# Kernel optimization log

Measured on AMD Instinct MI355X. Metric: run time of the kernel, lower is better.

The kernel has to match this reference:

```python
import jax, jax.numpy as jnp
import numpy as np

N = 100000      # nodes
E = 1600000     # edges (avg degree 16)
IN_FEATS = 128
HEADS = 4
OUT_FEATS = 16
NEG_SLOPE = 0.2
EPS = 1e-16


def setup_inputs() -> dict:
    key = jax.random.key(0)
    k1, k2, k3, k4, k5, k6 = jax.random.split(key, 6)
    feat = jax.random.normal(k1, (N, IN_FEATS), dtype=jnp.float32)
    # xavier-ish scale for params
    W = jax.random.normal(k2, (IN_FEATS, HEADS * OUT_FEATS), dtype=jnp.float32) * 0.1
    attn_l = jax.random.normal(k3, (1, HEADS, OUT_FEATS), dtype=jnp.float32) * 0.1
    attn_r = jax.random.normal(k4, (1, HEADS, OUT_FEATS), dtype=jnp.float32) * 0.1
    src_index = jax.random.randint(k5, (E,), 0, N, dtype=jnp.int32)
    trg_index = jax.random.randint(k6, (E,), 0, N, dtype=jnp.int32)
    return {"feat": feat, "W": W, "attn_l": attn_l, "attn_r": attn_r,
            "src_index": src_index, "trg_index": trg_index}


def reference(feat, W, attn_l, attn_r, src_index, trg_index):
    # dropout layers are identity in eval mode
    n = feat.shape[0]
    h = (feat @ W).reshape(n, HEADS, OUT_FEATS)            # [N,H,F]
    el = jnp.sum(h * attn_l, axis=-1)                      # [N,H]
    er = jnp.sum(h * attn_r, axis=-1)                      # [N,H]
    s = el[src_index] + er[trg_index]                      # [E,H] edge scores
    s = jnp.where(s > 0, s, NEG_SLOPE * s)                 # LeakyReLU(0.2)
    # neighborhood-aware softmax over incoming edges of each target node
    s = s - jnp.max(s)                                     # global max shift (as in source)
    e = jnp.exp(s)                                         # [E,H]
    denom = jax.ops.segment_sum(e, trg_index, num_segments=n)  # [N,H]
    attn = e / (denom[trg_index] + EPS)                    # [E,H]
    # weighted aggregation of lifted source features into target nodes
    msg = h[src_index] * attn[:, :, None]                  # [E,H,F]
    h_prime = jax.ops.segment_sum(msg, trg_index, num_segments=n)  # [N,H,F]
    return h_prime.reshape(n, HEADS * OUT_FEATS)
```

## Files before the change

kernel.cpp:

```cpp
#include <hip/hip_runtime.h>

typedef unsigned short ushort_t;
typedef __attribute__((ext_vector_type(8))) short bf16x8;
typedef __attribute__((ext_vector_type(4))) float f32x4v;

#define EPB 8000

static __device__ __forceinline__ float bf2f(ushort_t u) {
  union { unsigned int i; float f; } v; v.i = ((unsigned int)u) << 16; return v.f;
}
static __device__ __forceinline__ ushort_t f2bf(float f) {
  union { float f; unsigned int i; } v; v.f = f;
  unsigned int r = v.i + 0x7FFFu + ((v.i >> 16) & 1u);
  return (ushort_t)(r >> 16);
}
static __device__ __forceinline__ short f2bfs(float f) {
  return (short)f2bf(f);
}
static __device__ __forceinline__ float leaky(float s) {
  return s > 0.f ? s : 0.2f * s;
}

__global__ __launch_bounds__(256) void gat_packw(
    const float* __restrict__ W, ushort_t* __restrict__ wfrag)
{
  const int t = threadIdx.x;
  const int w = t >> 6, l = t & 63;
  const int q = l >> 4, n = l & 15;
  #pragma unroll
  for (int kc = 0; kc < 4; ++kc) {
    #pragma unroll
    for (int j = 0; j < 8; ++j) {
      const int k = kc * 32 + q * 8 + j;
      wfrag[(((w * 4 + kc) * 64) + l) * 8 + j] = f2bf(W[k * 64 + w * 16 + n]);
    }
  }
}

__global__ __launch_bounds__(256) void gat_linear(
    const float* __restrict__ feat, const ushort_t* __restrict__ wfrag,
    const float* __restrict__ attnl, const float* __restrict__ attnr,
    ushort_t* __restrict__ h_out, float* __restrict__ el, float* __restrict__ er,
    float* __restrict__ blockmax2, int N)
{
  __shared__ float sF[16 * 132];
  __shared__ float wmax[8];
  const int t = threadIdx.x;
  const int b = blockIdx.x;
  const int w = t >> 6, l = t & 63;
  const int q = l >> 4, m = l & 15;

  bf16x8 bfr[4];
  #pragma unroll
  for (int kc = 0; kc < 4; ++kc)
    bfr[kc] = *(const bf16x8*)(wfrag + (((w * 4 + kc) * 64) + l) * 8);

  const float al = attnl[w * 16 + m];
  const float ar = attnr[w * 16 + m];

  const float4* gF = (const float4*)(feat + (size_t)b * 16 * 128);
  #pragma unroll
  for (int i = 0; i < 2; ++i) {
    const int idx = i * 256 + t;
    const int node = idx >> 5, off = idx & 31;
    float4 v = make_float4(0.f, 0.f, 0.f, 0.f);
    if (b * 16 + node < N) v = gF[idx];
    *(float4*)(sF + node * 132 + off * 4) = v;
  }
  __syncthreads();

  f32x4v acc = {0.f, 0.f, 0.f, 0.f};
  const float* arow = sF + m * 132 + q * 8;
  #pragma unroll
  for (int kc = 0; kc < 4; ++kc) {
    const float4 a0 = *(const float4*)(arow + kc * 32);
    const float4 a1 = *(const float4*)(arow + kc * 32 + 4);
    bf16x8 af;
    af[0] = f2bfs(a0.x); af[1] = f2bfs(a0.y);
    af[2] = f2bfs(a0.z); af[3] = f2bfs(a0.w);
    af[4] = f2bfs(a1.x); af[5] = f2bfs(a1.y);
    af[6] = f2bfs(a1.z); af[7] = f2bfs(a1.w);
    acc = __builtin_amdgcn_mfma_f32_16x16x32_bf16(af, bfr[kc], acc, 0, 0, 0);
  }

  float mel = -1e30f, mer = -1e30f;
  #pragma unroll
  for (int r = 0; r < 4; ++r) {
    const int node = q * 4 + r;
    const int gn = b * 16 + node;
    const float hv = acc[r];
    float evl = hv * al;
    float evr = hv * ar;
    #pragma unroll
    for (int off = 8; off >= 1; off >>= 1) {
      evl += __shfl_xor(evl, off, 16);
      evr += __shfl_xor(evr, off, 16);
    }
    if (gn < N) {
      h_out[(size_t)gn * 64 + w * 16 + m] = f2bf(hv);
      if (m == 0) {
        el[gn * 4 + w] = evl;
        er[gn * 4 + w] = evr;
      }
    }
    mel = fmaxf(mel, evl);
    mer = fmaxf(mer, evr);
  }
  mel = fmaxf(mel, __shfl_xor(mel, 16, 64));
  mel = fmaxf(mel, __shfl_xor(mel, 32, 64));
  mer = fmaxf(mer, __shfl_xor(mer, 16, 64));
  mer = fmaxf(mer, __shfl_xor(mer, 32, 64));
  if (l == 0) { wmax[w * 2] = mel; wmax[w * 2 + 1] = mer; }
  __syncthreads();
  if (t == 0) {
    float a = fmaxf(fmaxf(wmax[0], wmax[2]), fmaxf(wmax[4], wmax[6]));
    float c = fmaxf(fmaxf(wmax[1], wmax[3]), fmaxf(wmax[5], wmax[7]));
    blockmax2[b * 2] = a;
    blockmax2[b * 2 + 1] = c;
  }
}

__global__ __launch_bounds__(256) void bucket_hist(
    const int* __restrict__ trg, int E, int nbkt, int* __restrict__ blockHist)
{
  __shared__ int hist[256];
  const int t = threadIdx.x, b = blockIdx.x;
  hist[t] = 0;
  __syncthreads();
  const int start = b * EPB;
  const int end = min(start + EPB, E);
  for (int e = start + t; e < end; e += 256)
    atomicAdd(&hist[trg[e] >> 9], 1);
  __syncthreads();
  if (t < nbkt) blockHist[b * nbkt + t] = hist[t];
}

__global__ __launch_bounds__(64) void bucket_scan(
    int* __restrict__ blockHist, int nb3, int nbkt, int* __restrict__ colTotal)
{
  const int b = blockIdx.x;
  const int l = threadIdx.x;
  int carry = 0;
  for (int r = 0; r * 64 < nb3; ++r) {
    const int i = r * 64 + l;
    int v = (i < nb3) ? blockHist[i * nbkt + b] : 0;
    int incl = v;
    #pragma unroll
    for (int d = 1; d < 64; d <<= 1) {
      int u = __shfl_up(incl, d, 64);
      if (l >= d) incl += u;
    }
    if (i < nb3) blockHist[i * nbkt + b] = carry + incl - v;
    carry += __shfl(incl, 63, 64);
  }
  if (l == 0) colTotal[b] = carry;
}

__global__ __launch_bounds__(256) void bucket_base(
    const int* __restrict__ colTotal, int nbkt, int* __restrict__ bucketBase,
    const float* __restrict__ blockmax2, int nbL, float* __restrict__ gmaxM,
    int* __restrict__ rowoff, int N, int E)
{
  const int t = threadIdx.x;
  const int l = t & 63, w = t >> 6;
  if (w == 0) {
    int carry = 0;
    for (int r = 0; r * 64 < nbkt; ++r) {
      const int i = r * 64 + l;
      int v = (i < nbkt) ? colTotal[i] : 0;
      int incl = v;
      #pragma unroll
      for (int d = 1; d < 64; d <<= 1) {
        int u = __shfl_up(incl, d, 64);
        if (l >= d) incl += u;
      }
      if (i < nbkt) bucketBase[i] = carry + incl - v;
      carry += __shfl(incl, 63, 64);
    }
    if (l == 0) { bucketBase[nbkt] = carry; rowoff[N] = E; }
  }
  float mel = -1e30f, mer = -1e30f;
  for (int i = t; i < nbL; i += 256) {
    mel = fmaxf(mel, blockmax2[i * 2]);
    mer = fmaxf(mer, blockmax2[i * 2 + 1]);
  }
  #pragma unroll
  for (int o = 32; o >= 1; o >>= 1) {
    mel = fmaxf(mel, __shfl_xor(mel, o, 64));
    mer = fmaxf(mer, __shfl_xor(mer, o, 64));
  }
  __shared__ float wm[8];
  if (l == 0) { wm[w * 2] = mel; wm[w * 2 + 1] = mer; }
  __syncthreads();
  if (t == 0) {
    float a = fmaxf(fmaxf(wm[0], wm[2]), fmaxf(wm[4], wm[6]));
    float c = fmaxf(fmaxf(wm[1], wm[3]), fmaxf(wm[5], wm[7]));
    gmaxM[0] = fmaxf(0.f, a + c);
  }
}

__global__ __launch_bounds__(256) void bucket_scatter(
    const int* __restrict__ src, const int* __restrict__ trg, int E, int nbkt,
    const int* __restrict__ blockHist, const int* __restrict__ bucketBase,
    unsigned int* __restrict__ binned)
{
  __shared__ int cursor[256];
  const int t = threadIdx.x, b = blockIdx.x;
  if (t < nbkt) cursor[t] = bucketBase[t] + blockHist[b * nbkt + t];
  __syncthreads();
  const int start = b * EPB;
  const int end = min(start + EPB, E);
  for (int e = start + t; e < end; e += 256) {
    const int ti = trg[e];
    const int bkt = ti >> 9;
    const int pos = atomicAdd(&cursor[bkt], 1);
    binned[pos] = ((unsigned int)src[e] << 9) | (unsigned int)(ti & 511);
  }
}

__global__ __launch_bounds__(512) void fine_scatter(
    const unsigned int* __restrict__ binned, const int* __restrict__ bucketBase,
    int* __restrict__ rowoff, int* __restrict__ csrsrc, int N)
{
  __shared__ int cnt[512];
  __shared__ int ws[8];
  const int t = threadIdx.x, b = blockIdx.x;
  const int l = t & 63, w = t >> 6;
  const int base = bucketBase[b];
  const int end = bucketBase[b + 1];
  cnt[t] = 0;
  __syncthreads();
  for (int i = base + t; i < end; i += 512)
    atomicAdd(&cnt[binned[i] & 511u], 1);
  __syncthreads();
  const int v = cnt[t];
  int incl = v;
  #pragma unroll
  for (int d = 1; d < 64; d <<= 1) {
    int u = __shfl_up(incl, d, 64);
    if (l >= d) incl += u;
  }
  if (l == 63) ws[w] = incl;
  __syncthreads();
  int woff = 0;
  for (int i = 0; i < w; ++i) woff += ws[i];
  const int loc = woff + incl - v;
  cnt[t] = loc;
  const int gt = b * 512 + t;
  if (gt < N) rowoff[gt] = base + loc;
  __syncthreads();
  for (int i = base + t; i < end; i += 512) {
    const unsigned int pv = binned[i];
    const int lt = (int)(pv & 511u);
    const int pos = base + atomicAdd(&cnt[lt], 1);
    csrsrc[pos] = (int)(pv >> 9);
  }
}

__global__ __launch_bounds__(256) void gat_agg(
    const int* __restrict__ csrsrc, const int* __restrict__ rowoff,
    const float4* __restrict__ el4, const float4* __restrict__ er4,
    const ushort_t* __restrict__ hbf, const float* __restrict__ gmaxM,
    float* __restrict__ out, int N)
{
  __shared__ float sP[4 * 64 * 4];
  const int t = threadIdx.x;
  const int l = t & 63;
  const int w = t >> 6;
  const int n = blockIdx.x * 4 + w;
  if (n >= N) return;
  const int hd = l >> 4;
  const int start = rowoff[n];
  const int end = rowoff[n + 1];
  const float M = gmaxM[0];
  const float4 ern = er4[n];
  float* sPw = sP + w * 256;

  float a0 = 0.f, a1 = 0.f, a2 = 0.f, a3 = 0.f;
  float dacc = 0.f;

  for (int base = start; base < end; base += 64) {
    const int cnt = min(64, end - base);
    int sn = 0;
    float4 pv = make_float4(0.f, 0.f, 0.f, 0.f);
    if (l < cnt) {
      sn = csrsrc[base + l];
      const float4 a = el4[sn];
      pv.x = __expf(leaky(a.x + ern.x) - M);
      pv.y = __expf(leaky(a.y + ern.y) - M);
      pv.z = __expf(leaky(a.z + ern.z) - M);
      pv.w = __expf(leaky(a.w + ern.w) - M);
    }
    *(float4*)(sPw + l * 4) = pv;

    int j = 0;
    for (; j + 4 <= cnt; j += 4) {
      const int s0 = __shfl(sn, j,     64);
      const int s1 = __shfl(sn, j + 1, 64);
      const int s2 = __shfl(sn, j + 2, 64);
      const int s3 = __shfl(sn, j + 3, 64);
      const float p0 = sPw[(j)     * 4 + hd];
      const float p1 = sPw[(j + 1) * 4 + hd];
      const float p2 = sPw[(j + 2) * 4 + hd];
      const float p3 = sPw[(j + 3) * 4 + hd];
      a0 += bf2f(hbf[(size_t)s0 * 64 + l]) * p0;
      a1 += bf2f(hbf[(size_t)s1 * 64 + l]) * p1;
      a2 += bf2f(hbf[(size_t)s2 * 64 + l]) * p2;
      a3 += bf2f(hbf[(size_t)s3 * 64 + l]) * p3;
      dacc += (p0 + p1) + (p2 + p3);
    }
    for (; j < cnt; ++j) {
      const int s0 = __shfl(sn, j, 64);
      const float p0 = sPw[j * 4 + hd];
      a0 += bf2f(hbf[(size_t)s0 * 64 + l]) * p0;
      dacc += p0;
    }
  }
  const float acc = (a0 + a1) + (a2 + a3);
  out[(size_t)n * 64 + l] = acc / (dacc + 1e-16f);
}

extern "C" void kernel_launch(void* const* d_in, const int* in_sizes, int n_in,
                              void* d_out, int out_size, void* d_ws, size_t ws_size,
                              hipStream_t stream) {
  const float* feat  = (const float*)d_in[0];
  const float* W     = (const float*)d_in[1];
  const float* attnl = (const float*)d_in[2];
  const float* attnr = (const float*)d_in[3];
  const int* src = (const int*)d_in[4];
  const int* trg = (const int*)d_in[5];
  float* out = (float*)d_out;

  const int N = in_sizes[0] / 128;
  const int E = in_sizes[4];

  const int nbL  = (N + 15) / 16;
  const int nbkt = (N + 511) >> 9;
  const int nb3  = (E + EPB - 1) / EPB;

  char* p = (char*)d_ws;
  auto take = [&](size_t bytes) -> char* {
    char* r = p;
    p += (bytes + 255) & ~(size_t)255;
    return r;
  };
  ushort_t* h_bf  = (ushort_t*)take((size_t)N * 64 * 2);
  float* el       = (float*)take((size_t)N * 16);
  float* er       = (float*)take((size_t)N * 16);
  int* rowoff     = (int*)take((size_t)(N + 1) * 4);
  int* csrsrc     = (int*)take((size_t)E * 4);
  unsigned int* binned = (unsigned int*)take((size_t)E * 4);
  ushort_t* wfrag = (ushort_t*)take(4 * 4 * 64 * 8 * 2);
  int* blockHist  = (int*)take((size_t)nb3 * nbkt * 4);
  int* colTotal   = (int*)take((size_t)nbkt * 4);
  int* bucketBase = (int*)take((size_t)(nbkt + 1) * 4);
  float* blockmax2 = (float*)take((size_t)nbL * 2 * 4);
  float* gmaxM    = (float*)take(256);

  gat_packw<<<1, 256, 0, stream>>>(W, wfrag);
  gat_linear<<<nbL, 256, 0, stream>>>(feat, wfrag, attnl, attnr,
                                      h_bf, el, er, blockmax2, N);
  bucket_hist<<<nb3, 256, 0, stream>>>(trg, E, nbkt, blockHist);
  bucket_scan<<<nbkt, 64, 0, stream>>>(blockHist, nb3, nbkt, colTotal);
  bucket_base<<<1, 256, 0, stream>>>(colTotal, nbkt, bucketBase,
                                     blockmax2, nbL, gmaxM, rowoff, N, E);
  bucket_scatter<<<nb3, 256, 0, stream>>>(src, trg, E, nbkt, blockHist,
                                          bucketBase, binned);
  fine_scatter<<<nbkt, 512, 0, stream>>>(binned, bucketBase, rowoff, csrsrc, N);
  gat_agg<<<(N + 3) / 4, 256, 0, stream>>>(csrsrc, rowoff, (const float4*)el,
                                           (const float4*)er, h_bf,
                                           gmaxM, out, N);
}
```

Baseline: 236.4 us.

## Fold attention vectors into W, fuse packing with histogram, widen linear tiles

W is pre-multiplied by attn_l/attn_r into a fifth MFMA tile, so el/er come straight out of the matmul instead of from shuffle reductions. Weight packing now runs as an extra block of the histogram kernel. The global-max reduction moves into fine_scatter and the linear kernel is launched later, cutting one launch and shrinking bucket_base. gat_linear now handles 64 nodes per block with bf16 staging in shared memory. The aggregation loop is unrolled to 8 accumulators with the softmax denominator summed per chunk via one cross-lane reduction. Folding attn into W in bf16 changes rounding of el/er.

```diff
diff --git a/kernel.cpp b/kernel.cpp
--- a/kernel.cpp
+++ b/kernel.cpp
@@ -14,117 +14,43 @@
   unsigned int r = v.i + 0x7FFFu + ((v.i >> 16) & 1u);
   return (ushort_t)(r >> 16);
 }
-static __device__ __forceinline__ short f2bfs(float f) {
-  return (short)f2bf(f);
-}
 static __device__ __forceinline__ float leaky(float s) {
   return s > 0.f ? s : 0.2f * s;
 }
 
-__global__ __launch_bounds__(256) void gat_packw(
-    const float* __restrict__ W, ushort_t* __restrict__ wfrag)
-{
+__global__ __launch_bounds__(256) void packw_hist(
+    const float* __restrict__ W, const float* __restrict__ attnl,
+    const float* __restrict__ attnr, ushort_t* __restrict__ wfrag,
+    const int* __restrict__ trg, int E, int nbkt,
+    int* __restrict__ blockHist, int nb3)
+{
+  const int b = blockIdx.x;
   const int t = threadIdx.x;
-  const int w = t >> 6, l = t & 63;
-  const int q = l >> 4, n = l & 15;
-  #pragma unroll
-  for (int kc = 0; kc < 4; ++kc) {
-    #pragma unroll
-    for (int j = 0; j < 8; ++j) {
-      const int k = kc * 32 + q * 8 + j;
-      wfrag[(((w * 4 + kc) * 64) + l) * 8 + j] = f2bf(W[k * 64 + w * 16 + n]);
-    }
-  }
-}
-
-__global__ __launch_bounds__(256) void gat_linear(
-    const float* __restrict__ feat, const ushort_t* __restrict__ wfrag,
-    const float* __restrict__ attnl, const float* __restrict__ attnr,
-    ushort_t* __restrict__ h_out, float* __restrict__ el, float* __restrict__ er,
-    float* __restrict__ blockmax2, int N)
-{
-  __shared__ float sF[16 * 132];
-  __shared__ float wmax[8];
-  const int t = threadIdx.x;
-  const int b = blockIdx.x;
-  const int w = t >> 6, l = t & 63;
-  const int q = l >> 4, m = l & 15;
-
-  bf16x8 bfr[4];
-  #pragma unroll
-  for (int kc = 0; kc < 4; ++kc)
-    bfr[kc] = *(const bf16x8*)(wfrag + (((w * 4 + kc) * 64) + l) * 8);
-
-  const float al = attnl[w * 16 + m];
-  const float ar = attnr[w * 16 + m];
-
-  const float4* gF = (const float4*)(feat + (size_t)b * 16 * 128);
-  #pragma unroll
-  for (int i = 0; i < 2; ++i) {
-    const int idx = i * 256 + t;
-    const int node = idx >> 5, off = idx & 31;
-    float4 v = make_float4(0.f, 0.f, 0.f, 0.f);
-    if (b * 16 + node < N) v = gF[idx];
-    *(float4*)(sF + node * 132 + off * 4) = v;
-  }
-  __syncthreads();
-
-  f32x4v acc = {0.f, 0.f, 0.f, 0.f};
-  const float* arow = sF + m * 132 + q * 8;
-  #pragma unroll
-  for (int kc = 0; kc < 4; ++kc) {
-    const float4 a0 = *(const float4*)(arow + kc * 32);
-    const float4 a1 = *(const float4*)(arow + kc * 32 + 4);
-    bf16x8 af;
-    af[0] = f2bfs(a0.x); af[1] = f2bfs(a0.y);
-    af[2] = f2bfs(a0.z); af[3] = f2bfs(a0.w);
-    af[4] = f2bfs(a1.x); af[5] = f2bfs(a1.y);
-    af[6] = f2bfs(a1.z); af[7] = f2bfs(a1.w);
-    acc = __builtin_amdgcn_mfma_f32_16x16x32_bf16(af, bfr[kc], acc, 0, 0, 0);
-  }
-
-  float mel = -1e30f, mer = -1e30f;
-  #pragma unroll
-  for (int r = 0; r < 4; ++r) {
-    const int node = q * 4 + r;
-    const int gn = b * 16 + node;
-    const float hv = acc[r];
-    float evl = hv * al;
-    float evr = hv * ar;
-    #pragma unroll
-    for (int off = 8; off >= 1; off >>= 1) {
-      evl += __shfl_xor(evl, off, 16);
-      evr += __shfl_xor(evr, off, 16);
-    }
-    if (gn < N) {
-      h_out[(size_t)gn * 64 + w * 16 + m] = f2bf(hv);
-      if (m == 0) {
-        el[gn * 4 + w] = evl;
-        er[gn * 4 + w] = evr;
+  if (b == nb3) {
+    const int kc = t >> 6, l = t & 63;
+    const int q = l >> 4, n = l & 15;
+    #pragma unroll
+    for (int tile = 0; tile < 5; ++tile) {
+      #pragma unroll
+      for (int j = 0; j < 8; ++j) {
+        const int k = kc * 32 + q * 8 + j;
+        float v = 0.f;
+        if (tile < 4) {
+          v = W[k * 64 + tile * 16 + n];
+        } else if (n < 4) {
+          for (int f = 0; f < 16; ++f)
+            v += W[k * 64 + n * 16 + f] * attnl[n * 16 + f];
+        } else if (n < 8) {
+          const int hd = n - 4;
+          for (int f = 0; f < 16; ++f)
+            v += W[k * 64 + hd * 16 + f] * attnr[hd * 16 + f];
+        }
+        wfrag[((tile * 4 + kc) * 64 + l) * 8 + j] = f2bf(v);
       }
     }
-    mel = fmaxf(mel, evl);
-    mer = fmaxf(mer, evr);
-  }
-  mel = fmaxf(mel, __shfl_xor(mel, 16, 64));
-  mel = fmaxf(mel, __shfl_xor(mel, 32, 64));
-  mer = fmaxf(mer, __shfl_xor(mer, 16, 64));
-  mer = fmaxf(mer, __shfl_xor(mer, 32, 64));
-  if (l == 0) { wmax[w * 2] = mel; wmax[w * 2 + 1] = mer; }
-  __syncthreads();
-  if (t == 0) {
-    float a = fmaxf(fmaxf(wmax[0], wmax[2]), fmaxf(wmax[4], wmax[6]));
-    float c = fmaxf(fmaxf(wmax[1], wmax[3]), fmaxf(wmax[5], wmax[7]));
-    blockmax2[b * 2] = a;
-    blockmax2[b * 2 + 1] = c;
-  }
-}
-
-__global__ __launch_bounds__(256) void bucket_hist(
-    const int* __restrict__ trg, int E, int nbkt, int* __restrict__ blockHist)
-{
+    return;
+  }
   __shared__ int hist[256];
-  const int t = threadIdx.x, b = blockIdx.x;
   hist[t] = 0;
   __syncthreads();
   const int start = b * EPB;
@@ -156,47 +82,25 @@
   if (l == 0) colTotal[b] = carry;
 }
 
-__global__ __launch_bounds__(256) void bucket_base(
+__global__ __launch_bounds__(64) void bucket_base(
     const int* __restrict__ colTotal, int nbkt, int* __restrict__ bucketBase,
-    const float* __restrict__ blockmax2, int nbL, float* __restrict__ gmaxM,
     int* __restrict__ rowoff, int N, int E)
 {
-  const int t = threadIdx.x;
-  const int l = t & 63, w = t >> 6;
-  if (w == 0) {
-    int carry = 0;
-    for (int r = 0; r * 64 < nbkt; ++r) {
-      const int i = r * 64 + l;
-      int v = (i < nbkt) ? colTotal[i] : 0;
-      int incl = v;
-      #pragma unroll
-      for (int d = 1; d < 64; d <<= 1) {
-        int u = __shfl_up(incl, d, 64);
-        if (l >= d) incl += u;
-      }
-      if (i < nbkt) bucketBase[i] = carry + incl - v;
-      carry += __shfl(incl, 63, 64);
-    }
-    if (l == 0) { bucketBase[nbkt] = carry; rowoff[N] = E; }
-  }
-  float mel = -1e30f, mer = -1e30f;
-  for (int i = t; i < nbL; i += 256) {
-    mel = fmaxf(mel, blockmax2[i * 2]);
-    mer = fmaxf(mer, blockmax2[i * 2 + 1]);
-  }
-  #pragma unroll
-  for (int o = 32; o >= 1; o >>= 1) {
-    mel = fmaxf(mel, __shfl_xor(mel, o, 64));
-    mer = fmaxf(mer, __shfl_xor(mer, o, 64));
-  }
-  __shared__ float wm[8];
-  if (l == 0) { wm[w * 2] = mel; wm[w * 2 + 1] = mer; }
-  __syncthreads();
-  if (t == 0) {
-    float a = fmaxf(fmaxf(wm[0], wm[2]), fmaxf(wm[4], wm[6]));
-    float c = fmaxf(fmaxf(wm[1], wm[3]), fmaxf(wm[5], wm[7]));
-    gmaxM[0] = fmaxf(0.f, a + c);
-  }
+  const int l = threadIdx.x;
+  int carry = 0;
+  for (int r = 0; r * 64 < nbkt; ++r) {
+    const int i = r * 64 + l;
+    int v = (i < nbkt) ? colTotal[i] : 0;
+    int incl = v;
+    #pragma unroll
+    for (int d = 1; d < 64; d <<= 1) {
+      int u = __shfl_up(incl, d, 64);
+      if (l >= d) incl += u;
+    }
+    if (i < nbkt) bucketBase[i] = carry + incl - v;
+    carry += __shfl(incl, 63, 64);
+  }
+  if (l == 0) { bucketBase[nbkt] = carry; rowoff[N] = E; }
 }
 
 __global__ __launch_bounds__(256) void bucket_scatter(
@@ -218,18 +122,121 @@
   }
 }
 
+__global__ __launch_bounds__(256) void gat_linear(
+    const float* __restrict__ feat, const ushort_t* __restrict__ wfrag,
+    ushort_t* __restrict__ h_out, float* __restrict__ el, float* __restrict__ er,
+    float* __restrict__ blockmax2, int N)
+{
+  __shared__ ushort_t sFb[64 * 136];
+  __shared__ float wmax[8];
+  const int t = threadIdx.x;
+  const int b = blockIdx.x;
+  const int w = t >> 6, l = t & 63;
+  const int q = l >> 4, m = l & 15;
+
+  const float4* gF = (const float4*)(feat + (size_t)b * 64 * 128);
+  #pragma unroll
+  for (int i = 0; i < 8; ++i) {
+    const int idx = i * 256 + t;
+    const int node = idx >> 5, off = idx & 31;
+    float4 v = make_float4(0.f, 0.f, 0.f, 0.f);
+    if (b * 64 + node < N) v = gF[idx];
+    unsigned int p0 = ((unsigned int)f2bf(v.y) << 16) | f2bf(v.x);
+    unsigned int p1 = ((unsigned int)f2bf(v.w) << 16) | f2bf(v.z);
+    *(uint2*)(sFb + node * 136 + off * 4) = make_uint2(p0, p1);
+  }
+  __syncthreads();
+
+  bf16x8 a[4];
+  const ushort_t* arow = sFb + (w * 16 + m) * 136 + q * 8;
+  #pragma unroll
+  for (int kc = 0; kc < 4; ++kc)
+    a[kc] = *(const bf16x8*)(arow + kc * 32);
+
+  #pragma unroll
+  for (int tile = 0; tile < 4; ++tile) {
+    f32x4v acc = {0.f, 0.f, 0.f, 0.f};
+    #pragma unroll
+    for (int kc = 0; kc < 4; ++kc) {
+      bf16x8 bfr = *(const bf16x8*)(wfrag + ((tile * 4 + kc) * 64 + l) * 8);
+      acc = __builtin_amdgcn_mfma_f32_16x16x32_bf16(a[kc], bfr, acc, 0, 0, 0);
+    }
+    #pragma unroll
+    for (int r = 0; r < 4; ++r) {
+      const int gn = b * 64 + w * 16 + q * 4 + r;
+      if (gn < N) h_out[(size_t)gn * 64 + tile * 16 + m] = f2bf(acc[r]);
+    }
+  }
+
+  f32x4v acc4 = {0.f, 0.f, 0.f, 0.f};
+  #pragma unroll
+  for (int kc = 0; kc < 4; ++kc) {
+    bf16x8 bfr = *(const bf16x8*)(wfrag + ((4 * 4 + kc) * 64 + l) * 8);
+    acc4 = __builtin_amdgcn_mfma_f32_16x16x32_bf16(a[kc], bfr, acc4, 0, 0, 0);
+  }
+  float mel = -1e30f, mer = -1e30f;
+  #pragma unroll
+  for (int r = 0; r < 4; ++r) {
+    const int gn = b * 64 + w * 16 + q * 4 + r;
+    const float v = acc4[r];
+    if (m < 4) {
+      if (gn < N) el[gn * 4 + m] = v;
+      mel = fmaxf(mel, v);
+    } else if (m < 8) {
+      if (gn < N) er[gn * 4 + (m - 4)] = v;
+      mer = fmaxf(mer, v);
+    }
+  }
+  #pragma unroll
+  for (int o = 1; o <= 32; o <<= 1) {
+    mel = fmaxf(mel, __shfl_xor(mel, o, 64));
+    mer = fmaxf(mer, __shfl_xor(mer, o, 64));
+  }
+  if (l == 0) { wmax[w * 2] = mel; wmax[w * 2 + 1] = mer; }
+  __syncthreads();
+  if (t == 0) {
+    float aa = fmaxf(fmaxf(wmax[0], wmax[2]), fmaxf(wmax[4], wmax[6]));
+    float cc = fmaxf(fmaxf(wmax[1], wmax[3]), fmaxf(wmax[5], wmax[7]));
+    blockmax2[b * 2] = aa;
+    blockmax2[b * 2 + 1] = cc;
+  }
+}
+
 __global__ __launch_bounds__(512) void fine_scatter(
     const unsigned int* __restrict__ binned, const int* __restrict__ bucketBase,
-    int* __restrict__ rowoff, int* __restrict__ csrsrc, int N)
+    int* __restrict__ rowoff, int* __restrict__ csrsrc, int N,
+    const float* __restrict__ blockmax2, int nbL, float* __restrict__ gmaxM)
 {
   __shared__ int cnt[512];
   __shared__ int ws[8];
+  __shared__ float wmg[16];
   const int t = threadIdx.x, b = blockIdx.x;
   const int l = t & 63, w = t >> 6;
   const int base = bucketBase[b];
   const int end = bucketBase[b + 1];
   cnt[t] = 0;
-  __syncthreads();
+  if (b == 0) {
+    float mel = -1e30f, mer = -1e30f;
+    for (int i = t; i < nbL; i += 512) {
+      mel = fmaxf(mel, blockmax2[i * 2]);
+      mer = fmaxf(mer, blockmax2[i * 2 + 1]);
+    }
+    #pragma unroll
+    for (int o = 1; o <= 32; o <<= 1) {
+      mel = fmaxf(mel, __shfl_xor(mel, o, 64));
+      mer = fmaxf(mer, __shfl_xor(mer, o, 64));
+    }
+    if (l == 0) { wmg[w * 2] = mel; wmg[w * 2 + 1] = mer; }
+  }
+  __syncthreads();
+  if (b == 0 && t == 0) {
+    float aa = -1e30f, cc = -1e30f;
+    for (int i = 0; i < 8; ++i) {
+      aa = fmaxf(aa, wmg[i * 2]);
+      cc = fmaxf(cc, wmg[i * 2 + 1]);
+    }
+    gmaxM[0] = fmaxf(0.f, aa + cc);
+  }
   for (int i = base + t; i < end; i += 512)
     atomicAdd(&cnt[binned[i] & 511u], 1);
   __syncthreads();
@@ -277,7 +284,8 @@
   float* sPw = sP + w * 256;
 
   float a0 = 0.f, a1 = 0.f, a2 = 0.f, a3 = 0.f;
-  float dacc = 0.f;
+  float a4 = 0.f, a5 = 0.f, a6 = 0.f, a7 = 0.f;
+  float4 dsum = make_float4(0.f, 0.f, 0.f, 0.f);
 
   for (int base = start; base < end; base += 64) {
     const int cnt = min(64, end - base);
@@ -291,32 +299,43 @@
       pv.z = __expf(leaky(a.z + ern.z) - M);
       pv.w = __expf(leaky(a.w + ern.w) - M);
     }
+    dsum.x += pv.x; dsum.y += pv.y; dsum.z += pv.z; dsum.w += pv.w;
     *(float4*)(sPw + l * 4) = pv;
 
     int j = 0;
-    for (; j + 4 <= cnt; j += 4) {
+    for (; j + 8 <= cnt; j += 8) {
       const int s0 = __shfl(sn, j,     64);
       const int s1 = __shfl(sn, j + 1, 64);
       const int s2 = __shfl(sn, j + 2, 64);
       const int s3 = __shfl(sn, j + 3, 64);
-      const float p0 = sPw[(j)     * 4 + hd];
-      const float p1 = sPw[(j + 1) * 4 + hd];
-      const float p2 = sPw[(j + 2) * 4 + hd];
-      const float p3 = sPw[(j + 3) * 4 + hd];
-      a0 += bf2f(hbf[(size_t)s0 * 64 + l]) * p0;
-      a1 += bf2f(hbf[(size_t)s1 * 64 + l]) * p1;
-      a2 += bf2f(hbf[(size_t)s2 * 64 + l]) * p2;
-      a3 += bf2f(hbf[(size_t)s3 * 64 + l]) * p3;
-      dacc += (p0 + p1) + (p2 + p3);
+      const int s4 = __shfl(sn, j + 4, 64);
+      const int s5 = __shfl(sn, j + 5, 64);
+      const int s6 = __shfl(sn, j + 6, 64);
+      const int s7 = __shfl(sn, j + 7, 64);
+      a0 += bf2f(hbf[(size_t)s0 * 64 + l]) * sPw[(j)     * 4 + hd];
+      a1 += bf2f(hbf[(size_t)s1 * 64 + l]) * sPw[(j + 1) * 4 + hd];
+      a2 += bf2f(hbf[(size_t)s2 * 64 + l]) * sPw[(j + 2) * 4 + hd];
+      a3 += bf2f(hbf[(size_t)s3 * 64 + l]) * sPw[(j + 3) * 4 + hd];
+      a4 += bf2f(hbf[(size_t)s4 * 64 + l]) * sPw[(j + 4) * 4 + hd];
+      a5 += bf2f(hbf[(size_t)s5 * 64 + l]) * sPw[(j + 5) * 4 + hd];
+      a6 += bf2f(hbf[(size_t)s6 * 64 + l]) * sPw[(j + 6) * 4 + hd];
+      a7 += bf2f(hbf[(size_t)s7 * 64 + l]) * sPw[(j + 7) * 4 + hd];
     }
     for (; j < cnt; ++j) {
       const int s0 = __shfl(sn, j, 64);
-      const float p0 = sPw[j * 4 + hd];
-      a0 += bf2f(hbf[(size_t)s0 * 64 + l]) * p0;
-      dacc += p0;
-    }
-  }
-  const float acc = (a0 + a1) + (a2 + a3);
+      a0 += bf2f(hbf[(size_t)s0 * 64 + l]) * sPw[j * 4 + hd];
+    }
+  }
+  #pragma unroll
+  for (int o = 1; o <= 32; o <<= 1) {
+    dsum.x += __shfl_xor(dsum.x, o, 64);
+    dsum.y += __shfl_xor(dsum.y, o, 64);
+    dsum.z += __shfl_xor(dsum.z, o, 64);
+    dsum.w += __shfl_xor(dsum.w, o, 64);
+  }
+  const float dacc = (hd == 0) ? dsum.x : (hd == 1) ? dsum.y
+                   : (hd == 2) ? dsum.z : dsum.w;
+  const float acc = ((a0 + a1) + (a2 + a3)) + ((a4 + a5) + (a6 + a7));
   out[(size_t)n * 64 + l] = acc / (dacc + 1e-16f);
 }
 
@@ -334,7 +353,7 @@
   const int N = in_sizes[0] / 128;
   const int E = in_sizes[4];
 
-  const int nbL  = (N + 15) / 16;
+  const int nbL  = (N + 63) / 64;
   const int nbkt = (N + 511) >> 9;
   const int nb3  = (E + EPB - 1) / EPB;
 
@@ -350,23 +369,23 @@
   int* rowoff     = (int*)take((size_t)(N + 1) * 4);
   int* csrsrc     = (int*)take((size_t)E * 4);
   unsigned int* binned = (unsigned int*)take((size_t)E * 4);
-  ushort_t* wfrag = (ushort_t*)take(4 * 4 * 64 * 8 * 2);
+  ushort_t* wfrag = (ushort_t*)take(5 * 4 * 64 * 8 * 2);
   int* blockHist  = (int*)take((size_t)nb3 * nbkt * 4);
   int* colTotal   = (int*)take((size_t)nbkt * 4);
   int* bucketBase = (int*)take((size_t)(nbkt + 1) * 4);
   float* blockmax2 = (float*)take((size_t)nbL * 2 * 4);
   float* gmaxM    = (float*)take(256);
 
-  gat_packw<<<1, 256, 0, stream>>>(W, wfrag);
-  gat_linear<<<nbL, 256, 0, stream>>>(feat, wfrag, attnl, attnr,
-                                      h_bf, el, er, blockmax2, N);
-  bucket_hist<<<nb3, 256, 0, stream>>>(trg, E, nbkt, blockHist);
+  packw_hist<<<nb3 + 1, 256, 0, stream>>>(W, attnl, attnr, wfrag,
+                                          trg, E, nbkt, blockHist, nb3);
   bucket_scan<<<nbkt, 64, 0, stream>>>(blockHist, nb3, nbkt, colTotal);
-  bucket_base<<<1, 256, 0, stream>>>(colTotal, nbkt, bucketBase,
-                                     blockmax2, nbL, gmaxM, rowoff, N, E);
+  bucket_base<<<1, 64, 0, stream>>>(colTotal, nbkt, bucketBase, rowoff, N, E);
   bucket_scatter<<<nb3, 256, 0, stream>>>(src, trg, E, nbkt, blockHist,
                                           bucketBase, binned);
-  fine_scatter<<<nbkt, 512, 0, stream>>>(binned, bucketBase, rowoff, csrsrc, N);
+  gat_linear<<<nbL, 256, 0, stream>>>(feat, wfrag, h_bf, el, er,
+                                      blockmax2, N);
+  fine_scatter<<<nbkt, 512, 0, stream>>>(binned, bucketBase, rowoff, csrsrc,
+                                         N, blockmax2, nbL, gmaxM);
   gat_agg<<<(N + 3) / 4, 256, 0, stream>>>(csrsrc, rowoff, (const float4*)el,
                                            (const float4*)er, h_bf,
                                            gmaxM, out, N);
```

Result: faster. 224.9 us (-4.9%).
